# Performance work log

Hardware: AMD Instinct MI355X
Metric: run time of the kernel (lower is better)

## Reference

```python
import jax, jax.numpy as jnp
import numpy as np

N_DRUG = 20000; N_DIS = 20000; E_G = 320000
B = 4096; N_MOL = 65536; E_MOL = 262144
IN = 128; H = 256; OUT = 128; NF = 9; V = 128
EPS = 1e-5


def _bn(x, g, b):
    # BatchNorm1d in training mode: batch statistics (biased var), eps=1e-5
    m = jnp.mean(x, 0); v = jnp.var(x, 0)
    return g * (x - m) * jax.lax.rsqrt(v + EPS) + b


def _gcn_conv(x, W, b, src, dst, n):
    # PyG GCNConv: add self-loops, sym-normalized aggregation of x@W, + bias
    h = x @ W  # [n, out]
    deg = jnp.ones((n,), x.dtype).at[dst].add(jnp.ones(src.shape, x.dtype))  # deg incl. self-loop
    dinv = jax.lax.rsqrt(deg)
    msg = (dinv[src] * dinv[dst])[:, None] * h[src]  # [E, out]
    out = (h / deg[:, None]).at[dst].add(msg)  # self-loop norm = 1/deg
    return out + b


def _gcn(x, Ws, bs, gs, betas, edge_index, n):
    src, dst = edge_index[0], edge_index[1]
    for i in range(len(Ws) - 1):
        x = jax.nn.relu(_bn(_gcn_conv(x, Ws[i], bs[i], src, dst, n), gs[i], betas[i]))
    return _gcn_conv(x, Ws[-1], bs[-1], src, dst, n)


def _conv_block(x, W, b, g, beta):
    # Conv1d(k=3,s=1,p=1) -> MaxPool1d(2,2) -> BatchNorm1d -> ReLU
    y = jax.lax.conv_general_dilated(x, W, (1,), ((1, 1),), dimension_numbers=('NCH', 'OIH', 'NCH')) + b[None, :, None]
    y = jax.lax.reduce_window(y, -jnp.inf, jax.lax.max, (1, 1, 2), (1, 1, 2), 'VALID')
    m = jnp.mean(y, (0, 2)); v = jnp.var(y, (0, 2))
    y = g[None, :, None] * (y - m[None, :, None]) * jax.lax.rsqrt(v + EPS)[None, :, None] + beta[None, :, None]
    return jax.nn.relu(y)


def setup_inputs() -> dict:
    key = jax.random.key(0)
    ks = iter(jax.random.split(key, 64))
    def nrm(shape, s=0.05):
        return jax.random.normal(next(ks), shape, jnp.float32) * s
    inp = {}
    inp['drug_x'] = nrm((N_DRUG, IN), 1.0)
    inp['drug_edge_index'] = jax.random.randint(next(ks), (2, E_G), 0, N_DRUG)
    inp['drug_idx'] = jax.random.randint(next(ks), (B,), 0, N_DRUG)
    inp['dis_x'] = nrm((N_DIS, IN), 1.0)
    inp['dis_edge_index'] = jax.random.randint(next(ks), (2, E_G), 0, N_DIS)
    inp['dis_idx'] = jax.random.randint(next(ks), (B,), 0, N_DIS)
    inp['mol_x'] = jax.random.randint(next(ks), (N_MOL, NF), 0, V)
    inp['mol_edge_index'] = jax.random.randint(next(ks), (2, E_MOL), 0, N_MOL)
    inp['mol_batch'] = jnp.sort(jax.random.randint(next(ks), (N_MOL,), 0, B))
    for p in ['dr', 'di']:
        inp[p + '_W0'] = nrm((IN, H)); inp[p + '_W1'] = nrm((H, H)); inp[p + '_W2'] = nrm((H, OUT))
        inp[p + '_b0'] = jnp.zeros((H,)); inp[p + '_b1'] = jnp.zeros((H,)); inp[p + '_b2'] = jnp.zeros((OUT,))
        inp[p + '_g0'] = jnp.ones((H,)); inp[p + '_g1'] = jnp.ones((H,))
        inp[p + '_be0'] = jnp.zeros((H,)); inp[p + '_be1'] = jnp.zeros((H,))
    inp['mol_emb'] = nrm((NF, V, H))
    inp['mo_W0'] = nrm((H, H)); inp['mo_W1'] = nrm((H, H)); inp['mo_W2'] = nrm((H, OUT))
    inp['mo_b0'] = jnp.zeros((H,)); inp['mo_b1'] = jnp.zeros((H,)); inp['mo_b2'] = jnp.zeros((OUT,))
    inp['mo_g0'] = jnp.ones((H,)); inp['mo_g1'] = jnp.ones((H,))
    inp['mo_be0'] = jnp.zeros((H,)); inp['mo_be1'] = jnp.zeros((H,))
    inp['c1_W'] = nrm((6, 3, 3), 0.2); inp['c1_b'] = jnp.zeros((6,)); inp['c1_g'] = jnp.ones((6,)); inp['c1_be'] = jnp.zeros((6,))
    inp['c2_W'] = nrm((6, 6, 3), 0.2); inp['c2_b'] = jnp.zeros((6,)); inp['c2_g'] = jnp.ones((6,)); inp['c2_be'] = jnp.zeros((6,))
    inp['l1_W'] = nrm((192, 128)); inp['l1_b'] = jnp.zeros((128,))
    inp['l2_W'] = nrm((128, 1)); inp['l2_b'] = jnp.zeros((1,))
    return inp


def reference(drug_x, drug_edge_index, drug_idx, dis_x, dis_edge_index, dis_idx, mol_x, mol_edge_index, mol_batch,
              dr_W0, dr_W1, dr_W2, dr_b0, dr_b1, dr_b2, dr_g0, dr_g1, dr_be0, dr_be1,
              di_W0, di_W1, di_W2, di_b0, di_b1, di_b2, di_g0, di_g1, di_be0, di_be1,
              mol_emb, mo_W0, mo_W1, mo_W2, mo_b0, mo_b1, mo_b2, mo_g0, mo_g1, mo_be0, mo_be1,
              c1_W, c1_b, c1_g, c1_be, c2_W, c2_b, c2_g, c2_be, l1_W, l1_b, l2_W, l2_b):
    dfeat = _gcn(drug_x, [dr_W0, dr_W1, dr_W2], [dr_b0, dr_b1, dr_b2], [dr_g0, dr_g1], [dr_be0, dr_be1], drug_edge_index, N_DRUG)
    sfeat = _gcn(dis_x, [di_W0, di_W1, di_W2], [di_b0, di_b1, di_b2], [di_g0, di_g1], [di_be0, di_be1], dis_edge_index, N_DIS)
    # AtomEncoder: sum of per-feature categorical embeddings -> [N_MOL, H]
    h = jnp.sum(mol_emb[jnp.arange(NF)[None, :], mol_x], axis=1)
    mfeat = _gcn(h, [mo_W0, mo_W1, mo_W2], [mo_b0, mo_b1, mo_b2], [mo_g0, mo_g1], [mo_be0, mo_be1], mol_edge_index, N_MOL)
    mpool = jax.ops.segment_sum(mfeat, mol_batch, num_segments=B)  # global_add_pool
    fea = jnp.concatenate([dfeat[drug_idx], mpool, sfeat[dis_idx]], axis=1).reshape(B, 3, OUT)
    fea = _conv_block(fea, c1_W, c1_b, c1_g, c1_be)
    fea = _conv_block(fea, c2_W, c2_b, c2_g, c2_be)
    fea = fea.reshape(B, -1)  # [B, 192]
    fea = jax.nn.relu(fea @ l1_W + l1_b)
    return fea @ l2_W + l2_b
```

## Files before the change

kernel.cpp:

```cpp
#include <hip/hip_runtime.h>
#include <hip/hip_bf16.h>

#define N_DRUG 20000
#define N_DIS  20000
#define E_G    320000
#define BATCH  4096
#define N_MOL  65536
#define E_MOL  262144
#define DIN    128
#define DH     256
#define NF     9
#define NV     128
#define SPAN_P 20096
#define NP     40192

typedef short s16x8 __attribute__((ext_vector_type(8)));
typedef unsigned short u16x8 __attribute__((ext_vector_type(8)));
typedef float f32x4 __attribute__((ext_vector_type(4)));

typedef __attribute__((address_space(1))) const void gvoid_t;
typedef __attribute__((address_space(3))) void lvoid_t;

__device__ __forceinline__ float bfu2f(unsigned short u) {
    return __uint_as_float(((unsigned int)u) << 16);
}
__device__ __forceinline__ unsigned short f2bfu(float f) {
    __hip_bfloat16 b = __float2bfloat16(f);
    return *reinterpret_cast<unsigned short*>(&b);
}
__device__ __forceinline__ void atomAddF(float* p, float v) { unsafeAtomicAdd(p, v); }

__global__ void k_sentinel(float* out, int n, float v) {
    int i = blockIdx.x * 256 + threadIdx.x;
    if (i < n) out[i] = v;
}

__global__ void k_cast_pair(const float* __restrict__ a, const float* __restrict__ b,
                            unsigned short* __restrict__ out) {
    int i4 = blockIdx.x * 256 + threadIdx.x;
    if (i4 >= NP * 32) return;
    int row = i4 >> 5, c4 = (i4 & 31) * 4;
    float4 v = {0.f, 0.f, 0.f, 0.f};
    if (row < N_DRUG) v = *reinterpret_cast<const float4*>(a + (size_t)row * 128 + c4);
    else if (row >= SPAN_P && row < SPAN_P + N_DIS)
        v = *reinterpret_cast<const float4*>(b + (size_t)(row - SPAN_P) * 128 + c4);
    ushort4 o = {f2bfu(v.x), f2bfu(v.y), f2bfu(v.z), f2bfu(v.w)};
    *reinterpret_cast<ushort4*>(out + (size_t)row * 128 + c4) = o;
}

__global__ void k_wcast3(const float* __restrict__ W0, const float* __restrict__ W1,
                         const float* __restrict__ W2,
                         unsigned short* __restrict__ T0, unsigned short* __restrict__ T1,
                         unsigned short* __restrict__ T2, int Cin) {
    int i = blockIdx.x * 256 + threadIdx.x;
    int t0 = Cin * 256, t1 = 256 * 256, t2 = 256 * 128;
    if (i < t0) {
        int k = i / 256, c = i - k * 256;
        T0[(size_t)c * Cin + k] = f2bfu(W0[i]);
    } else if (i < t0 + t1) {
        int e = i - t0;
        int k = e / 256, c = e - k * 256;
        T1[(size_t)c * 256 + k] = f2bfu(W1[e]);
    } else if (i < t0 + t1 + t2) {
        int e = i - t0 - t1;
        int k = e / 128, c = e - k * 128;
        T2[(size_t)c * 256 + k] = f2bfu(W2[e]);
    }
}

__global__ void k_count(const int* __restrict__ dst, int* __restrict__ cnt, int E) {
    int e = blockIdx.x * 256 + threadIdx.x;
    if (e < E) atomicAdd(&cnt[dst[e]], 1);
}
__global__ void k_count2(const int* __restrict__ eiA, const int* __restrict__ eiB,
                         int* __restrict__ cnt) {
    int e = blockIdx.x * 256 + threadIdx.x;
    if (e >= 2 * E_G) return;
    int d = (e < E_G) ? eiA[E_G + e] : eiB[E_G + e - E_G] + SPAN_P;
    atomicAdd(&cnt[d], 1);
}

__global__ void k_scan1(const int* __restrict__ cnt, int* __restrict__ rowStart,
                        int* __restrict__ bsum, float* __restrict__ dinv, int n) {
    __shared__ int sh[256];
    int i = blockIdx.x * 256 + threadIdx.x;
    int v = (i < n) ? cnt[i] : 0;
    if (i < n) dinv[i] = rsqrtf(1.0f + (float)v);
    sh[threadIdx.x] = v;
    __syncthreads();
    for (int off = 1; off < 256; off <<= 1) {
        int t = (threadIdx.x >= off) ? sh[threadIdx.x - off] : 0;
        __syncthreads();
        sh[threadIdx.x] += t;
        __syncthreads();
    }
    if (i < n) rowStart[i] = sh[threadIdx.x] - v;
    if (threadIdx.x == 255) bsum[blockIdx.x] = sh[255];
}
__global__ void k_scan3(int* __restrict__ rowStart, int* __restrict__ cursor,
                        const int* __restrict__ bsum, int n, int nb, int E) {
    __shared__ int sh[256];
    int t = threadIdx.x;
    int v = (t < nb) ? bsum[t] : 0;
    sh[t] = v;
    __syncthreads();
    for (int off = 1; off < 256; off <<= 1) {
        int u = (t >= off) ? sh[t - off] : 0;
        __syncthreads();
        sh[t] += u;
        __syncthreads();
    }
    int pre = (blockIdx.x == 0) ? 0 : sh[blockIdx.x - 1];
    int i = blockIdx.x * 256 + t;
    if (i < n) {
        int r = rowStart[i] + pre;
        rowStart[i] = r;
        cursor[i] = r;
    }
    if (i == 0) rowStart[n] = E;
}
__global__ void k_fill(const int* __restrict__ src, const int* __restrict__ dst,
                       const float* __restrict__ dinv,
                       int* __restrict__ cursor, int2* __restrict__ csr2, int E) {
    int e = blockIdx.x * 256 + threadIdx.x;
    if (e < E) {
        int s = src[e], d = dst[e];
        int p = atomicAdd(&cursor[d], 1);
        csr2[p] = make_int2(s, __float_as_int(dinv[s] * dinv[d]));
    }
}
__global__ void k_fill2(const int* __restrict__ eiA, const int* __restrict__ eiB,
                        const float* __restrict__ dinv,
                        int* __restrict__ cursor, int2* __restrict__ csr2) {
    int e = blockIdx.x * 256 + threadIdx.x;
    if (e >= 2 * E_G) return;
    int s, d;
    if (e < E_G) { s = eiA[e]; d = eiA[E_G + e]; }
    else { s = eiB[e - E_G] + SPAN_P; d = eiB[E_G + e - E_G] + SPAN_P; }
    int p = atomicAdd(&cursor[d], 1);
    csr2[p] = make_int2(s, __float_as_int(dinv[s] * dinv[d]));
}

template<int AFFINE, int STATS, int BATCHED>
__global__ __launch_bounds__(256) void k_gemm_mfma(const unsigned short* __restrict__ A,
                                                   const unsigned short* __restrict__ Bt0,
                                                   const unsigned short* __restrict__ Bt1,
                                                   const float* __restrict__ coef,
                                                   unsigned short* __restrict__ Cout,
                                                   float* __restrict__ bnbuf,
                                                   int Mloc, int SPAN, int K, int N) {
    __shared__ unsigned short Al[2][4][128][8];
    __shared__ unsigned short Bl[2][4][128][8];
    __shared__ float csc[256], csh[256];
    const int tid = threadIdx.x;
    const int bm = blockIdx.y * 128;
    const int bn = blockIdx.x * 128;
    int g, lbm;
    if (BATCHED) { int tpg = SPAN >> 7; g = (int)blockIdx.y / tpg; lbm = bm - g * SPAN; }
    else { g = 0; lbm = bm; }
    const unsigned short* Bt = g ? Bt1 : Bt0;
    const int w = tid >> 6, l = tid & 63;
    const int wrow = (w >> 1) * 64, wcol = (w & 1) * 64;
    const int kg = l >> 4, lr = l & 15;

    if (AFFINE) {
        for (int i = tid; i < K; i += 256) {
            csc[i] = coef[g * 512 + i];
            csh[i] = coef[g * 512 + 256 + i];
        }
    }
    if (lbm + 128 > Mloc) {
        for (int s = tid; s < 1024; s += 256) {
            u16x8 z = {0, 0, 0, 0, 0, 0, 0, 0};
            *reinterpret_cast<u16x8*>(&Al[0][0][0][0] + s * 8) = z;
        }
    }
    __syncthreads();

    auto stage = [&](int buf, int k0) {
#pragma unroll
        for (int i = 0; i < 4; ++i) {
            int id = w * 4 + i;
            int koff = (id >> 1) & 3;
            int half = id & 1;
            int row = half * 64 + l;
            if (id < 8) {
                if (lbm + row < Mloc) {
                    const unsigned short* gs = A + (size_t)(bm + row) * K + k0 + koff * 8;
                    __builtin_amdgcn_global_load_lds((gvoid_t*)gs,
                        (lvoid_t*)&Al[buf][koff][half * 64][0], 16, 0, 0);
                }
            } else {
                const unsigned short* gs = Bt + (size_t)(bn + row) * K + k0 + koff * 8;
                __builtin_amdgcn_global_load_lds((gvoid_t*)gs,
                    (lvoid_t*)&Bl[buf][koff][half * 64][0], 16, 0, 0);
            }
        }
    };

    f32x4 acc[4][4];
#pragma unroll
    for (int fm = 0; fm < 4; ++fm)
#pragma unroll
        for (int fn = 0; fn < 4; ++fn) acc[fm][fn] = f32x4{0.f, 0.f, 0.f, 0.f};

    stage(0, 0);
    __syncthreads();
    int nk = K >> 5;
    for (int t = 0; t < nk; ++t) {
        int cur = t & 1;
        if (t + 1 < nk) stage(cur ^ 1, (t + 1) * 32);
        s16x8 a[4], b[4];
#pragma unroll
        for (int fm = 0; fm < 4; ++fm)
            a[fm] = *reinterpret_cast<const s16x8*>(&Al[cur][kg][wrow + fm * 16 + lr][0]);
        if (AFFINE) {
            int k0 = t * 32;
            float sc[8], sh[8];
#pragma unroll
            for (int e = 0; e < 8; ++e) {
                sc[e] = csc[k0 + kg * 8 + e];
                sh[e] = csh[k0 + kg * 8 + e];
            }
#pragma unroll
            for (int fm = 0; fm < 4; ++fm)
#pragma unroll
                for (int e = 0; e < 8; ++e) {
// ... 12 lines not shown
        __syncthreads();
    }
#pragma unroll
    for (int fm = 0; fm < 4; ++fm)
#pragma unroll
        for (int r = 0; r < 4; ++r) {
            int row = bm + wrow + fm * 16 + kg * 4 + r;
#pragma unroll
            for (int fn = 0; fn < 4; ++fn) {
                int col = bn + wcol + fn * 16 + lr;
                Cout[(size_t)row * N + col] = f2bfu(acc[fm][fn][r]);
            }
        }
    if constexpr (STATS) {
        __shared__ float colS[128], colQ[128];
        if (tid < 128) { colS[tid] = 0.f; colQ[tid] = 0.f; }
        __syncthreads();
#pragma unroll
        for (int fn = 0; fn < 4; ++fn) {
            float s = 0.f, q = 0.f;
#pragma unroll
            for (int fm = 0; fm < 4; ++fm)
#pragma unroll
                for (int r = 0; r < 4; ++r) {
                    float v = acc[fm][fn][r];
                    s += v; q += v * v;
                }
            int cl = (w & 1) * 64 + fn * 16 + lr;
            atomicAdd(&colS[cl], s);
            atomicAdd(&colQ[cl], q);
        }
        __syncthreads();
        if (tid < 128) {
            atomAddF(&bnbuf[g * 512 + bn + tid], colS[tid]);
            atomAddF(&bnbuf[g * 512 + 256 + bn + tid], colQ[tid]);
        }
    }
}

template<int C, int BIAS, int OUTBF>
__global__ __launch_bounds__(256) void k_gather(const unsigned short* __restrict__ h,
                                                const float* __restrict__ dinv,
                                                const float* __restrict__ bias0,
                                                const float* __restrict__ bias1,
                                                const int2* __restrict__ csr2,
                                                const int* __restrict__ rowStart,
                                                void* __restrict__ outv, int n, int SPAN) {
    constexpr int PL = C / 32;
    int row = blockIdx.x * 8 + (threadIdx.x >> 5);
    if (row >= n) return;
    int lane = threadIdx.x & 31;
    int c0 = lane * PL;

    auto loadRow = [&](int r, float* d) {
        const unsigned short* base = h + (size_t)r * C + c0;
        if constexpr (PL == 8) {
            u16x8 v = *reinterpret_cast<const u16x8*>(base);
#pragma unroll
            for (int e = 0; e < 8; ++e) d[e] = bfu2f((unsigned short)v[e]);
        } else {
            ushort4 v = *reinterpret_cast<const ushort4*>(base);
            d[0] = bfu2f(v.x); d[1] = bfu2f(v.y); d[2] = bfu2f(v.z); d[3] = bfu2f(v.w);
        }
    };

    float dd = dinv[row], ws = dd * dd;
    int beg = rowStart[row], end = rowStart[row + 1];
    float a0[PL], a1[PL], a2[PL], a3[PL], t0[PL], t1[PL], t2[PL], t3[PL];
    loadRow(row, t0);
#pragma unroll
    for (int p = 0; p < PL; ++p) { a0[p] = t0[p] * ws; a1[p] = 0.f; a2[p] = 0.f; a3[p] = 0.f; }

    int j = beg;
    for (; j + 4 <= end; j += 4) {
        int2 e0 = csr2[j], e1 = csr2[j + 1], e2 = csr2[j + 2], e3 = csr2[j + 3];
        float w0 = __int_as_float(e0.y), w1 = __int_as_float(e1.y);
        float w2 = __int_as_float(e2.y), w3 = __int_as_float(e3.y);
        loadRow(e0.x, t0); loadRow(e1.x, t1); loadRow(e2.x, t2); loadRow(e3.x, t3);
#pragma unroll
        for (int p = 0; p < PL; ++p) {
            a0[p] += w0 * t0[p]; a1[p] += w1 * t1[p];
            a2[p] += w2 * t2[p]; a3[p] += w3 * t3[p];
        }
    }
    for (; j < end; ++j) {
        int2 e0 = csr2[j];
        float w = __int_as_float(e0.y);
        loadRow(e0.x, t0);
#pragma unroll
        for (int p = 0; p < PL; ++p) a0[p] += w * t0[p];
    }
    const float* bp = (BIAS && row >= SPAN) ? bias1 : bias0;
#pragma unroll
    for (int p = 0; p < PL; ++p) {
        a0[p] += (a1[p] + a2[p]) + a3[p];
        if (BIAS) a0[p] += bp[c0 + p];
    }
    if constexpr (OUTBF) {
        unsigned short* o = (unsigned short*)outv + (size_t)row * C + c0;
        if constexpr (PL == 8) {
            u16x8 ov;
#pragma unroll
            for (int e = 0; e < 8; ++e) ov[e] = f2bfu(a0[e]);
            *reinterpret_cast<u16x8*>(o) = ov;
        } else {
            ushort4 ov = {f2bfu(a0[0]), f2bfu(a0[1]), f2bfu(a0[2]), f2bfu(a0[3])};
            *reinterpret_cast<ushort4*>(o) = ov;
        }
    } else {
        float* o = (float*)outv + (size_t)row * C + c0;
#pragma unroll
        for (int q = 0; q < PL / 4; ++q) {
            float4 ov = {a0[q * 4 + 0], a0[q * 4 + 1], a0[q * 4 + 2], a0[q * 4 + 3]};
            *reinterpret_cast<float4*>(o + q * 4) = ov;
        }
    }
}

__global__ __launch_bounds__(256) void k_bn_stats_bf(const unsigned short* __restrict__ x,
                                                     float* __restrict__ bnbuf, int SPAN) {
    __shared__ float smS[8][256];
    __shared__ float smQ[8][256];
    int t = threadIdx.x;
    int y = blockIdx.y;
    int g = t >> 5;
    int lane = t & 31;
    int c0 = lane * 8;
    float s[8], q[8];
#pragma unroll
    for (int e = 0; e < 8; ++e) { s[e] = 0.f; q[e] = 0.f; }
    int stride = gridDim.x * 8;
    for (int r = blockIdx.x * 8 + g; r < SPAN; r += stride) {
        u16x8 v = *reinterpret_cast<const u16x8*>(x + ((size_t)y * SPAN + r) * 256 + c0);
#pragma unroll
        for (int e = 0; e < 8; ++e) {
            float f = bfu2f((unsigned short)v[e]);
            s[e] += f; q[e] += f * f;
        }
    }
#pragma unroll
    for (int e = 0; e < 8; ++e) { smS[g][c0 + e] = s[e]; smQ[g][c0 + e] = q[e]; }
    __syncthreads();
    float S = 0.f, Q = 0.f;
#pragma unroll
    for (int g2 = 0; g2 < 8; ++g2) { S += smS[g2][t]; Q += smQ[g2][t]; }
    atomAddF(&bnbuf[y * 512 + t], S);
    atomAddF(&bnbuf[y * 512 + 256 + t], Q);
}

__global__ void k_bn_coef(float* __restrict__ bnbuf,
                          const float* __restrict__ gA, const float* __restrict__ beA,
                          const float* __restrict__ gB, const float* __restrict__ beB,
                          float* __restrict__ coef, float invN) {
    int gg = blockIdx.x;
    int j = threadIdx.x;
    const float* gp = gg ? gB : gA;
    const float* bp = gg ? beB : beA;
    float* s = bnbuf + gg * 512;
    float m = s[j] * invN;
    float v = s[256 + j] * invN - m * m;
    float r = rsqrtf(fmaxf(v, 0.f) + 1e-5f);
    float sc = gp[j] * r;
    coef[gg * 512 + j] = sc;
    coef[gg * 512 + 256 + j] = bp[j] - m * sc;
    s[j] = 0.f;
    s[256 + j] = 0.f;
}

__global__ __launch_bounds__(256) void k_atom_enc(const int* __restrict__ mol_x,
                                                  const float* __restrict__ emb,
                                                  unsigned short* __restrict__ h) {
    __shared__ int sidx[4][NF];
    int t = threadIdx.x;
    if (t < 4 * NF) sidx[t / NF][t % NF] = mol_x[(blockIdx.x * 4 + t / NF) * NF + t % NF];
    __syncthreads();
    int r = t >> 6, lane = t & 63;
    int c0 = lane * 4;
    int row = blockIdx.x * 4 + r;
    float4 s = {0.f, 0.f, 0.f, 0.f};
#pragma unroll
    for (int f = 0; f < NF; ++f) {
        const float4 v = *reinterpret_cast<const float4*>(emb + ((size_t)f * NV + sidx[r][f]) * DH + c0);
        s.x += v.x; s.y += v.y; s.z += v.z; s.w += v.w;
    }
    ushort4 ov = {f2bfu(s.x), f2bfu(s.y), f2bfu(s.z), f2bfu(s.w)};
    *reinterpret_cast<ushort4*>(h + (size_t)row * DH + c0) = ov;
}

__global__ __launch_bounds__(128) void k_pool_seg(const unsigned short* __restrict__ mfeat,
                                                  const int* __restrict__ batch,
                                                  float* __restrict__ mpool) {
    __shared__ int sr[2];
    __shared__ float smS[8][128];
    int b = blockIdx.x, t = threadIdx.x;
    if (t < 2) {
        int target = b + t;
        int lo = 0, hi = N_MOL;
        while (lo < hi) {
            int mid = (lo + hi) >> 1;
            if (batch[mid] < target) lo = mid + 1; else hi = mid;
        }
        sr[t] = lo;
    }
    __syncthreads();
    int g = t >> 4;
    int lane = t & 15;
    int c0 = lane * 8;
    float s[8];
#pragma unroll
    for (int e = 0; e < 8; ++e) s[e] = 0.f;
    int e1 = sr[1];
    for (int i = sr[0] + g; i < e1; i += 8) {
        u16x8 v = *reinterpret_cast<const u16x8*>(mfeat + (size_t)i * 128 + c0);
#pragma unroll
        for (int e = 0; e < 8; ++e) s[e] += bfu2f((unsigned short)v[e]);
    }
#pragma unroll
    for (int e = 0; e < 8; ++e) smS[g][c0 + e] = s[e];
    __syncthreads();
    float S = 0.f;
#pragma unroll
    for (int g2 = 0; g2 < 8; ++g2) S += smS[g2][t];
    mpool[(size_t)b * 128 + t] = S;
}

__global__ __launch_bounds__(64) void k_conv1(const float* __restrict__ dfeat,
                                              const float* __restrict__ mpool,
                                              const float* __restrict__ sfeat,
                                              const int* __restrict__ drug_idx,
                                              const int* __restrict__ dis_idx,
                                              const float* __restrict__ W,
                                              const float* __restrict__ bias,
                                              float* __restrict__ y1) {
    __shared__ float xs[3][128];
    __shared__ float w[54];
    __shared__ float bb[6];
    int b = blockIdx.x, t = threadIdx.x;
    int di = drug_idx[b], si = dis_idx[b];
    const float* r0 = dfeat + (size_t)di * 128;
    const float* r1 = mpool + (size_t)b * 128;
    const float* r2 = sfeat + (size_t)si * 128;
    xs[0][t] = r0[t]; xs[0][t + 64] = r0[t + 64];
    xs[1][t] = r1[t]; xs[1][t + 64] = r1[t + 64];
    xs[2][t] = r2[t]; xs[2][t + 64] = r2[t + 64];
    if (t < 54) w[t] = W[t];
    if (t < 6) bb[t] = bias[t];
    __syncthreads();
    int l0 = 2 * t, l1 = l0 + 1;
// ... 102 lines not shown
                                              const float* __restrict__ l1b,
                                              const float* __restrict__ l2W,
                                              const float* __restrict__ l2b,
                                              float* __restrict__ out) {
    __shared__ float fs[192];
    __shared__ float sm[2];
    int b = blockIdx.x, t = threadIdx.x;
    const float* mean = hb + 32 + 16;
    const float* rstd = hb + 32 + 24;
    for (int idx = t; idx < 192; idx += 128) {
        int o = idx >> 5, l = idx & 31;
        float v = y2[((size_t)b * 6 + o) * 32 + l];
        v = g2[o] * (v - mean[o]) * rstd[o] + be2[o];
        fs[idx] = fmaxf(v, 0.f);
    }
    __syncthreads();
    float h = l1b[t];
    for (int k = 0; k < 192; ++k)
        h += fs[k] * l1W[k * 128 + t];
    h = fmaxf(h, 0.f);
    float p = h * l2W[t];
#pragma unroll
    for (int off = 32; off > 0; off >>= 1) p += __shfl_down(p, off);
    if ((t & 63) == 0) sm[t >> 6] = p;
    __syncthreads();
    if (t == 0) out[b] = sm[0] + sm[1] + l2b[0];
}

extern "C" void kernel_launch(void* const* d_in, const int* in_sizes, int n_in,
                              void* d_out, int out_size, void* d_ws, size_t ws_size,
                              hipStream_t stream) {
    float* out = (float*)d_out;
    if (n_in != 52) { k_sentinel<<<16, 256, 0, stream>>>(out, out_size, -111.f); return; }
    if (in_sizes[0] != N_DRUG * DIN || in_sizes[29] != NF * NV * DH || in_sizes[48] != 192 * 128) {
        k_sentinel<<<16, 256, 0, stream>>>(out, out_size, -222.f); return;
    }

    char* w = (char*)d_ws;
    auto alloc = [&](size_t bytes) { char* p = w; w += (bytes + 255) & ~(size_t)255; return p; };
    unsigned short* xb    = (unsigned short*)alloc((size_t)N_MOL * 256 * 2);
    unsigned short* h_bf  = (unsigned short*)alloc((size_t)N_MOL * 256 * 2);
    unsigned short* xin   = (unsigned short*)alloc((size_t)N_MOL * 256 * 2);
    float* outDS = (float*)alloc((size_t)NP * 128 * 4);
    float* mpool = (float*)alloc((size_t)BATCH * 128 * 4);
    int*   cnt      = (int*)alloc((size_t)N_MOL * 4);
    float* dinv     = (float*)alloc((size_t)N_MOL * 4);
    int*   rowStart = (int*)alloc((size_t)(N_MOL + 1) * 4);
    int*   cursor   = (int*)alloc((size_t)N_MOL * 4);
    int2*  csr2     = (int2*)alloc((size_t)(2 * E_G) * 8);
    int*   bsum     = (int*)alloc(512 * 4);
    float* bnbuf    = (float*)alloc(1024 * 4);
    float* coef     = (float*)alloc(1024 * 4);
    unsigned short* wtA0 = (unsigned short*)alloc((size_t)256 * 256 * 2);
    unsigned short* wtA1 = (unsigned short*)alloc((size_t)256 * 256 * 2);
    unsigned short* wtA2 = (unsigned short*)alloc((size_t)256 * 256 * 2);
    unsigned short* wtB0 = (unsigned short*)alloc((size_t)256 * 256 * 2);
    unsigned short* wtB1 = (unsigned short*)alloc((size_t)256 * 256 * 2);
    unsigned short* wtB2 = (unsigned short*)alloc((size_t)256 * 256 * 2);
    float* hstat = (float*)alloc(64 * 4);
    float* y1    = (float*)alloc((size_t)BATCH * 6 * 64 * 4);
    float* y2    = (float*)alloc((size_t)BATCH * 6 * 32 * 4);
    if ((size_t)(w - (char*)d_ws) > ws_size) {
        k_sentinel<<<16, 256, 0, stream>>>(out, out_size, -333.f); return;
    }

    const float* drug_x  = (const float*)d_in[0];
    const int* drug_ei   = (const int*)d_in[1];
    const int* drug_idx  = (const int*)d_in[2];
    const float* dis_x   = (const float*)d_in[3];
    const int* dis_ei    = (const int*)d_in[4];
    const int* dis_idx   = (const int*)d_in[5];
    const int* mol_x     = (const int*)d_in[6];
    const int* mol_ei    = (const int*)d_in[7];
    const int* mol_b     = (const int*)d_in[8];
    const float *dr_W0 = (const float*)d_in[9], *dr_W1 = (const float*)d_in[10], *dr_W2 = (const float*)d_in[11];
    const float *dr_b2 = (const float*)d_in[14];
    const float *dr_g0 = (const float*)d_in[15], *dr_g1 = (const float*)d_in[16];
    const float *dr_be0 = (const float*)d_in[17], *dr_be1 = (const float*)d_in[18];
    const float *di_W0 = (const float*)d_in[19], *di_W1 = (const float*)d_in[20], *di_W2 = (const float*)d_in[21];
    const float *di_b2 = (const float*)d_in[24];
    const float *di_g0 = (const float*)d_in[25], *di_g1 = (const float*)d_in[26];
    const float *di_be0 = (const float*)d_in[27], *di_be1 = (const float*)d_in[28];
    const float* mol_emb = (const float*)d_in[29];
    const float *mo_W0 = (const float*)d_in[30], *mo_W1 = (const float*)d_in[31], *mo_W2 = (const float*)d_in[32];
    const float *mo_b2 = (const float*)d_in[35];
    const float *mo_g0 = (const float*)d_in[36], *mo_g1 = (const float*)d_in[37];
    const float *mo_be0 = (const float*)d_in[38], *mo_be1 = (const float*)d_in[39];
    const float *c1_W = (const float*)d_in[40], *c1_b = (const float*)d_in[41];
    const float *c1_g = (const float*)d_in[42], *c1_be = (const float*)d_in[43];
    const float *c2_W = (const float*)d_in[44], *c2_b = (const float*)d_in[45];
    const float *c2_g = (const float*)d_in[46], *c2_be = (const float*)d_in[47];
    const float *l1_W = (const float*)d_in[48], *l1_b = (const float*)d_in[49];
    const float *l2_W = (const float*)d_in[50], *l2_b = (const float*)d_in[51];

    hipMemsetAsync(bnbuf, 0, 1024 * sizeof(float), stream);
    float invNP = 1.0f / (float)N_DRUG;
    float invNM = 1.0f / (float)N_MOL;

    k_cast_pair<<<(NP * 32 + 255) / 256, 256, 0, stream>>>(drug_x, dis_x, xin);
    hipMemsetAsync(cnt, 0, (size_t)NP * sizeof(int), stream);
    k_count2<<<(2 * E_G + 255) / 256, 256, 0, stream>>>(drug_ei, dis_ei, cnt);
    int nbP = (NP + 255) / 256;
    k_scan1<<<nbP, 256, 0, stream>>>(cnt, rowStart, bsum, dinv, NP);
    k_scan3<<<nbP, 256, 0, stream>>>(rowStart, cursor, bsum, NP, nbP, 2 * E_G);
    k_fill2<<<(2 * E_G + 255) / 256, 256, 0, stream>>>(drug_ei, dis_ei, dinv, cursor, csr2);
    int wtot = 128 * 256 + 256 * 256 + 256 * 128;
    k_wcast3<<<(wtot + 255) / 256, 256, 0, stream>>>(dr_W0, dr_W1, dr_W2, wtA0, wtA1, wtA2, 128);
    k_wcast3<<<(wtot + 255) / 256, 256, 0, stream>>>(di_W0, di_W1, di_W2, wtB0, wtB1, wtB2, 128);

    int gbP = NP / 8;
    int tyP = NP / 128;
    k_gather<128, 0, 1><<<gbP, 256, 0, stream>>>(xin, dinv, nullptr, nullptr, csr2, rowStart, xb, NP, SPAN_P);
    k_gemm_mfma<0, 1, 1><<<dim3(2, tyP), 256, 0, stream>>>(xb, wtA0, wtB0, nullptr, h_bf, bnbuf, N_DRUG, SPAN_P, 128, 256);
    k_bn_coef<<<2, 256, 0, stream>>>(bnbuf, dr_g0, dr_be0, di_g0, di_be0, coef, invNP);
    k_gemm_mfma<1, 0, 1><<<dim3(2, tyP), 256, 0, stream>>>(h_bf, wtA1, wtB1, coef, xb, nullptr, N_DRUG, SPAN_P, 256, 256);
    k_gather<256, 0, 1><<<gbP, 256, 0, stream>>>(xb, dinv, nullptr, nullptr, csr2, rowStart, h_bf, NP, SPAN_P);
    k_bn_stats_bf<<<dim3(256, 2), 256, 0, stream>>>(h_bf, bnbuf, SPAN_P);
    k_bn_coef<<<2, 256, 0, stream>>>(bnbuf, dr_g1, dr_be1, di_g1, di_be1, coef, invNP);
    k_gemm_mfma<1, 0, 1><<<dim3(1, tyP), 256, 0, stream>>>(h_bf, wtA2, wtB2, coef, xb, nullptr, N_DRUG, SPAN_P, 256, 128);
    k_gather<128, 1, 0><<<gbP, 256, 0, stream>>>(xb, dinv, dr_b2, di_b2, csr2, rowStart, outDS, NP, SPAN_P);

    k_atom_enc<<<N_MOL / 4, 256, 0, stream>>>(mol_x, mol_emb, xin);
    hipMemsetAsync(cnt, 0, (size_t)N_MOL * sizeof(int), stream);
    k_count<<<(E_MOL + 255) / 256, 256, 0, stream>>>(mol_ei + E_MOL, cnt, E_MOL);
    int nbM = N_MOL / 256;
    k_scan1<<<nbM, 256, 0, stream>>>(cnt, rowStart, bsum, dinv, N_MOL);
    k_scan3<<<nbM, 256, 0, stream>>>(rowStart, cursor, bsum, N_MOL, nbM, E_MOL);
    k_fill<<<(E_MOL + 255) / 256, 256, 0, stream>>>(mol_ei, mol_ei + E_MOL, dinv, cursor, csr2, E_MOL);
    int wtotM = 256 * 256 + 256 * 256 + 256 * 128;
    k_wcast3<<<(wtotM + 255) / 256, 256, 0, stream>>>(mo_W0, mo_W1, mo_W2, wtA0, wtA1, wtA2, 256);

    int gbM = N_MOL / 8;
    int tyM = N_MOL / 128;
    k_gather<256, 0, 1><<<gbM, 256, 0, stream>>>(xin, dinv, nullptr, nullptr, csr2, rowStart, xb, N_MOL, N_MOL);
    k_gemm_mfma<0, 1, 0><<<dim3(2, tyM), 256, 0, stream>>>(xb, wtA0, wtA0, nullptr, h_bf, bnbuf, N_MOL, N_MOL, 256, 256);
    k_bn_coef<<<1, 256, 0, stream>>>(bnbuf, mo_g0, mo_be0, mo_g0, mo_be0, coef, invNM);
    k_gemm_mfma<1, 0, 0><<<dim3(2, tyM), 256, 0, stream>>>(h_bf, wtA1, wtA1, coef, xb, nullptr, N_MOL, N_MOL, 256, 256);
    k_gather<256, 0, 1><<<gbM, 256, 0, stream>>>(xb, dinv, nullptr, nullptr, csr2, rowStart, h_bf, N_MOL, N_MOL);
    k_bn_stats_bf<<<dim3(256, 1), 256, 0, stream>>>(h_bf, bnbuf, N_MOL);
    k_bn_coef<<<1, 256, 0, stream>>>(bnbuf, mo_g1, mo_be1, mo_g1, mo_be1, coef, invNM);
    k_gemm_mfma<1, 0, 0><<<dim3(1, tyM), 256, 0, stream>>>(h_bf, wtA2, wtA2, coef, xb, nullptr, N_MOL, N_MOL, 256, 128);
    k_gather<128, 1, 1><<<gbM, 256, 0, stream>>>(xb, dinv, mo_b2, mo_b2, csr2, rowStart, h_bf, N_MOL, N_MOL);
    k_pool_seg<<<BATCH, 128, 0, stream>>>(h_bf, mol_b, mpool);

    const float* dfeat = outDS;
    const float* sfeat = outDS + (size_t)SPAN_P * 128;
    hipMemsetAsync(hstat, 0, 64 * 4, stream);
    k_conv1<<<BATCH, 64, 0, stream>>>(dfeat, mpool, sfeat, drug_idx, dis_idx, c1_W, c1_b, y1);
    k_head_stats<<<dim3(6, BATCH / 256), 256, 0, stream>>>(y1, hstat, 0, 64);
    k_bn_fin<<<1, 8, 0, stream>>>(hstat, 0, 1.0f / (BATCH * 64.0f));
    k_conv2<<<BATCH, 64, 0, stream>>>(y1, hstat, c1_g, c1_be, c2_W, c2_b, y2);
    k_head_stats<<<dim3(6, BATCH / 256), 256, 0, stream>>>(y2, hstat, 1, 32);
    k_bn_fin<<<1, 8, 0, stream>>>(hstat, 1, 1.0f / (BATCH * 32.0f));
    k_head<<<BATCH, 128, 0, stream>>>(y2, hstat, c2_g, c2_be, l1_W, l1_b, l2_W, l2_b, out);
}
```

Before: 596.2 us.

## Batch drug, disease and molecule GCNs into shared launches over a concatenated graph

Concatenates the drug, disease and molecule graphs into one node and edge space so CSR build, gathers, GEMMs and BN stats/coef run as combined launches covering all three GCNs. This cuts the number of kernel launches and lets the small drug/disease work overlap with the larger molecule work instead of running serially. The final layer output now stays in fp32 for all graphs, so pooling reads float instead of bf16, which adds memory traffic. The combined scan also adds a separate block-sum scan kernel.

Measured after the change: 561.8 us. 5.8% less time.

```diff
diff --git a/kernel.cpp b/kernel.cpp
--- a/kernel.cpp
+++ b/kernel.cpp
@@ -7,12 +7,13 @@
 #define BATCH  4096
 #define N_MOL  65536
 #define E_MOL  262144
-#define DIN    128
-#define DH     256
 #define NF     9
 #define NV     128
+#define DH     256
 #define SPAN_P 20096
 #define NP     40192
+#define NTOT   105728
+#define ETOT   902144
 
 typedef short s16x8 __attribute__((ext_vector_type(8)));
 typedef unsigned short u16x8 __attribute__((ext_vector_type(8)));
@@ -68,15 +69,14 @@
     }
 }
 
-__global__ void k_count(const int* __restrict__ dst, int* __restrict__ cnt, int E) {
+__global__ void k_count3(const int* __restrict__ eA, const int* __restrict__ eB,
+                         const int* __restrict__ eC, int* __restrict__ cnt) {
     int e = blockIdx.x * 256 + threadIdx.x;
-    if (e < E) atomicAdd(&cnt[dst[e]], 1);
-}
-__global__ void k_count2(const int* __restrict__ eiA, const int* __restrict__ eiB,
-                         int* __restrict__ cnt) {
-    int e = blockIdx.x * 256 + threadIdx.x;
-    if (e >= 2 * E_G) return;
-    int d = (e < E_G) ? eiA[E_G + e] : eiB[E_G + e - E_G] + SPAN_P;
+    if (e >= ETOT) return;
+    int d;
+    if (e < E_G) d = eA[E_G + e];
+    else if (e < 2 * E_G) d = eB[E_G + (e - E_G)] + SPAN_P;
+    else d = eC[E_MOL + (e - 2 * E_G)] + NP;
     atomicAdd(&cnt[d], 1);
 }
 
@@ -97,76 +97,83 @@
     if (i < n) rowStart[i] = sh[threadIdx.x] - v;
     if (threadIdx.x == 255) bsum[blockIdx.x] = sh[255];
 }
+__global__ void k_scan2b(int* __restrict__ bsum, int nb) {
+    __shared__ int sh[256];
+    __shared__ int carry;
+    int t = threadIdx.x;
+    if (t == 0) carry = 0;
+    __syncthreads();
+    for (int c0 = 0; c0 < nb; c0 += 256) {
+        int v = (c0 + t < nb) ? bsum[c0 + t] : 0;
+        sh[t] = v;
+        __syncthreads();
+        for (int off = 1; off < 256; off <<= 1) {
+            int u = (t >= off) ? sh[t - off] : 0;
+            __syncthreads();
+            sh[t] += u;
+            __syncthreads();
+        }
+        if (c0 + t < nb) bsum[c0 + t] = carry + sh[t] - v;
+        __syncthreads();
+        if (t == 0) carry += sh[255];
+        __syncthreads();
+    }
+}
 __global__ void k_scan3(int* __restrict__ rowStart, int* __restrict__ cursor,
-                        const int* __restrict__ bsum, int n, int nb, int E) {
-    __shared__ int sh[256];
-    int t = threadIdx.x;
-    int v = (t < nb) ? bsum[t] : 0;
-    sh[t] = v;
-    __syncthreads();
-    for (int off = 1; off < 256; off <<= 1) {
-        int u = (t >= off) ? sh[t - off] : 0;
-        __syncthreads();
-        sh[t] += u;
-        __syncthreads();
-    }
-    int pre = (blockIdx.x == 0) ? 0 : sh[blockIdx.x - 1];
-    int i = blockIdx.x * 256 + t;
+                        const int* __restrict__ bsum, int n, int E) {
+    int i = blockIdx.x * 256 + threadIdx.x;
     if (i < n) {
-        int r = rowStart[i] + pre;
+        int r = rowStart[i] + bsum[blockIdx.x];
         rowStart[i] = r;
         cursor[i] = r;
     }
     if (i == 0) rowStart[n] = E;
 }
-__global__ void k_fill(const int* __restrict__ src, const int* __restrict__ dst,
-                       const float* __restrict__ dinv,
-                       int* __restrict__ cursor, int2* __restrict__ csr2, int E) {
-    int e = blockIdx.x * 256 + threadIdx.x;
-    if (e < E) {
-        int s = src[e], d = dst[e];
-        int p = atomicAdd(&cursor[d], 1);
-        csr2[p] = make_int2(s, __float_as_int(dinv[s] * dinv[d]));
-    }
-}
-__global__ void k_fill2(const int* __restrict__ eiA, const int* __restrict__ eiB,
-                        const float* __restrict__ dinv,
+__global__ void k_fill3(const int* __restrict__ eA, const int* __restrict__ eB,
+                        const int* __restrict__ eC, const float* __restrict__ dinv,
                         int* __restrict__ cursor, int2* __restrict__ csr2) {
     int e = blockIdx.x * 256 + threadIdx.x;
-    if (e >= 2 * E_G) return;
+    if (e >= ETOT) return;
     int s, d;
-    if (e < E_G) { s = eiA[e]; d = eiA[E_G + e]; }
-    else { s = eiB[e - E_G] + SPAN_P; d = eiB[E_G + e - E_G] + SPAN_P; }
+    if (e < E_G) { s = eA[e]; d = eA[E_G + e]; }
+    else if (e < 2 * E_G) { int i = e - E_G; s = eB[i] + SPAN_P; d = eB[E_G + i] + SPAN_P; }
+    else { int i = e - 2 * E_G; s = eC[i] + NP; d = eC[E_MOL + i] + NP; }
     int p = atomicAdd(&cursor[d], 1);
     csr2[p] = make_int2(s, __float_as_int(dinv[s] * dinv[d]));
 }
 
-template<int AFFINE, int STATS, int BATCHED>
+template<int AFFINE, int STATS>
 __global__ __launch_bounds__(256) void k_gemm_mfma(const unsigned short* __restrict__ A,
                                                    const unsigned short* __restrict__ Bt0,
                                                    const unsigned short* __restrict__ Bt1,
+                                                   const unsigned short* __restrict__ Bt2,
                                                    const float* __restrict__ coef,
                                                    unsigned short* __restrict__ Cout,
                                                    float* __restrict__ bnbuf,
-                                                   int Mloc, int SPAN, int K, int N) {
+                                                   int tb0, int tb1, int off1, int off2,
+                                                   int m0, int m1, int m2, int gbase,
+                                                   int K, int N) {
     __shared__ unsigned short Al[2][4][128][8];
     __shared__ unsigned short Bl[2][4][128][8];
     __shared__ float csc[256], csh[256];
     const int tid = threadIdx.x;
-    const int bm = blockIdx.y * 128;
+    const int y = blockIdx.y;
+    const int bm = y * 128;
     const int bn = blockIdx.x * 128;
-    int g, lbm;
-    if (BATCHED) { int tpg = SPAN >> 7; g = (int)blockIdx.y / tpg; lbm = bm - g * SPAN; }
-    else { g = 0; lbm = bm; }
-    const unsigned short* Bt = g ? Bt1 : Bt0;
+    const int g = (y >= tb1) ? 2 : ((y >= tb0) ? 1 : 0);
+    const int off = (g == 0) ? 0 : ((g == 1) ? off1 : off2);
+    const int Mloc = (g == 0) ? m0 : ((g == 1) ? m1 : m2);
+    const int lbm = bm - off;
+    const unsigned short* Bt = (g == 0) ? Bt0 : ((g == 1) ? Bt1 : Bt2);
+    const int gs = gbase + g;
     const int w = tid >> 6, l = tid & 63;
     const int wrow = (w >> 1) * 64, wcol = (w & 1) * 64;
     const int kg = l >> 4, lr = l & 15;
 
     if (AFFINE) {
         for (int i = tid; i < K; i += 256) {
-            csc[i] = coef[g * 512 + i];
-            csh[i] = coef[g * 512 + 256 + i];
+            csc[i] = coef[gs * 512 + i];
+            csh[i] = coef[gs * 512 + 256 + i];
         }
     }
     if (lbm + 128 > Mloc) {
@@ -186,13 +193,13 @@
             int row = half * 64 + l;
             if (id < 8) {
                 if (lbm + row < Mloc) {
-                    const unsigned short* gs = A + (size_t)(bm + row) * K + k0 + koff * 8;
-                    __builtin_amdgcn_global_load_lds((gvoid_t*)gs,
+                    const unsigned short* gsrc = A + (size_t)(bm + row) * K + k0 + koff * 8;
+                    __builtin_amdgcn_global_load_lds((gvoid_t*)gsrc,
                         (lvoid_t*)&Al[buf][koff][half * 64][0], 16, 0, 0);
                 }
             } else {
-                const unsigned short* gs = Bt + (size_t)(bn + row) * K + k0 + koff * 8;
-                __builtin_amdgcn_global_load_lds((gvoid_t*)gs,
+                const unsigned short* gsrc = Bt + (size_t)(bn + row) * K + k0 + koff * 8;
+                __builtin_amdgcn_global_load_lds((gvoid_t*)gsrc,
                     (lvoid_t*)&Bl[buf][koff][half * 64][0], 16, 0, 0);
             }
         }
@@ -271,28 +278,31 @@
         }
         __syncthreads();
         if (tid < 128) {
-            atomAddF(&bnbuf[g * 512 + bn + tid], colS[tid]);
-            atomAddF(&bnbuf[g * 512 + 256 + bn + tid], colQ[tid]);
+            atomAddF(&bnbuf[gs * 512 + bn + tid], colS[tid]);
+            atomAddF(&bnbuf[gs * 512 + 256 + bn + tid], colQ[tid]);
         }
     }
 }
 
 template<int C, int BIAS, int OUTBF>
 __global__ __launch_bounds__(256) void k_gather(const unsigned short* __restrict__ h,
+                                                long long hoff,
                                                 const float* __restrict__ dinv,
-                                                const float* __restrict__ bias0,
-                                                const float* __restrict__ bias1,
+                                                const float* __restrict__ b0,
+                                                const float* __restrict__ b1,
+                                                const float* __restrict__ b2,
                                                 const int2* __restrict__ csr2,
                                                 const int* __restrict__ rowStart,
-                                                void* __restrict__ outv, int n, int SPAN) {
+                                                void* __restrict__ outv, long long ooff,
+                                                int rowoff, int rowend) {
     constexpr int PL = C / 32;
-    int row = blockIdx.x * 8 + (threadIdx.x >> 5);
-    if (row >= n) return;
+    int row = rowoff + blockIdx.x * 8 + (threadIdx.x >> 5);
+    if (row >= rowend) return;
     int lane = threadIdx.x & 31;
     int c0 = lane * PL;
 
     auto loadRow = [&](int r, float* d) {
-        const unsigned short* base = h + (size_t)r * C + c0;
+        const unsigned short* base = h + ((size_t)r * C - hoff) + c0;
         if constexpr (PL == 8) {
             u16x8 v = *reinterpret_cast<const u16x8*>(base);
 #pragma unroll
@@ -329,14 +339,15 @@
 #pragma unroll
         for (int p = 0; p < PL; ++p) a0[p] += w * t0[p];
     }
-    const float* bp = (BIAS && row >= SPAN) ? bias1 : bias0;
+    const float* bp = nullptr;
+    if (BIAS) bp = (row < SPAN_P) ? b0 : ((row < NP) ? b1 : b2);
 #pragma unroll
     for (int p = 0; p < PL; ++p) {
         a0[p] += (a1[p] + a2[p]) + a3[p];
         if (BIAS) a0[p] += bp[c0 + p];
     }
     if constexpr (OUTBF) {
-        unsigned short* o = (unsigned short*)outv + (size_t)row * C + c0;
+        unsigned short* o = (unsigned short*)outv + ((size_t)row * C - ooff) + c0;
         if constexpr (PL == 8) {
             u16x8 ov;
 #pragma unroll
@@ -347,7 +358,7 @@
             *reinterpret_cast<ushort4*>(o) = ov;
         }
     } else {
-        float* o = (float*)outv + (size_t)row * C + c0;
+        float* o = (float*)outv + ((size_t)row * C - ooff) + c0;
 #pragma unroll
         for (int q = 0; q < PL / 4; ++q) {
             float4 ov = {a0[q * 4 + 0], a0[q * 4 + 1], a0[q * 4 + 2], a0[q * 4 + 3]};
@@ -356,12 +367,14 @@
     }
 }
 
-__global__ __launch_bounds__(256) void k_bn_stats_bf(const unsigned short* __restrict__ x,
-                                                     float* __restrict__ bnbuf, int SPAN) {
+__global__ __launch_bounds__(256) void k_bn_stats3(const unsigned short* __restrict__ x,
+                                                   float* __restrict__ bnbuf) {
     __shared__ float smS[8][256];
     __shared__ float smQ[8][256];
     int t = threadIdx.x;
     int y = blockIdx.y;
+    int off = (y < 2) ? y * SPAN_P : NP;
+    int span = (y < 2) ? SPAN_P : N_MOL;
     int g = t >> 5;
     int lane = t & 31;
     int c0 = lane * 8;
@@ -369,8 +382,8 @@
 #pragma unroll
     for (int e = 0; e < 8; ++e) { s[e] = 0.f; q[e] = 0.f; }
     int stride = gridDim.x * 8;
-    for (int r = blockIdx.x * 8 + g; r < SPAN; r += stride) {
-        u16x8 v = *reinterpret_cast<const u16x8*>(x + ((size_t)y * SPAN + r) * 256 + c0);
+    for (int r = blockIdx.x * 8 + g; r < span; r += stride) {
+        u16x8 v = *reinterpret_cast<const u16x8*>(x + ((size_t)(off + r)) * 256 + c0);
 #pragma unroll
         for (int e = 0; e < 8; ++e) {
             float f = bfu2f((unsigned short)v[e]);
@@ -387,14 +400,16 @@
     atomAddF(&bnbuf[y * 512 + 256 + t], Q);
 }
 
-__global__ void k_bn_coef(float* __restrict__ bnbuf,
-                          const float* __restrict__ gA, const float* __restrict__ beA,
-                          const float* __restrict__ gB, const float* __restrict__ beB,
-                          float* __restrict__ coef, float invN) {
+__global__ void k_bn_coef3(float* __restrict__ bnbuf,
+                           const float* __restrict__ g0, const float* __restrict__ be0,
+                           const float* __restrict__ g1, const float* __restrict__ be1,
+                           const float* __restrict__ g2, const float* __restrict__ be2,
+                           float* __restrict__ coef, float invN01, float invN2) {
     int gg = blockIdx.x;
     int j = threadIdx.x;
-    const float* gp = gg ? gB : gA;
-    const float* bp = gg ? beB : beA;
+    const float* gp = (gg == 0) ? g0 : ((gg == 1) ? g1 : g2);
+    const float* bp = (gg == 0) ? be0 : ((gg == 1) ? be1 : be2);
+    float invN = (gg < 2) ? invN01 : invN2;
     float* s = bnbuf + gg * 512;
     float m = s[j] * invN;
     float v = s[256 + j] * invN - m * m;
@@ -426,9 +441,9 @@
     *reinterpret_cast<ushort4*>(h + (size_t)row * DH + c0) = ov;
 }
 
-__global__ __launch_bounds__(128) void k_pool_seg(const unsigned short* __restrict__ mfeat,
-                                                  const int* __restrict__ batch,
-                                                  float* __restrict__ mpool) {
+__global__ __launch_bounds__(128) void k_pool_seg_f(const float* __restrict__ mfeat,
+                                                    const int* __restrict__ batch,
+                                                    float* __restrict__ mpool) {
     __shared__ int sr[2];
     __shared__ float smS[8][128];
     int b = blockIdx.x, t = threadIdx.x;
@@ -450,9 +465,10 @@
     for (int e = 0; e < 8; ++e) s[e] = 0.f;
     int e1 = sr[1];
     for (int i = sr[0] + g; i < e1; i += 8) {
-        u16x8 v = *reinterpret_cast<const u16x8*>(mfeat + (size_t)i * 128 + c0);
-#pragma unroll
-        for (int e = 0; e < 8; ++e) s[e] += bfu2f((unsigned short)v[e]);
+        const float4 v0 = *reinterpret_cast<const float4*>(mfeat + (size_t)i * 128 + c0);
+        const float4 v1 = *reinterpret_cast<const float4*>(mfeat + (size_t)i * 128 + c0 + 4);
+        s[0] += v0.x; s[1] += v0.y; s[2] += v0.z; s[3] += v0.w;
+        s[4] += v1.x; s[5] += v1.y; s[6] += v1.z; s[7] += v1.w;
     }
 #pragma unroll
     for (int e = 0; e < 8; ++e) smS[g][c0 + e] = s[e];
@@ -621,31 +637,33 @@
                               hipStream_t stream) {
     float* out = (float*)d_out;
     if (n_in != 52) { k_sentinel<<<16, 256, 0, stream>>>(out, out_size, -111.f); return; }
-    if (in_sizes[0] != N_DRUG * DIN || in_sizes[29] != NF * NV * DH || in_sizes[48] != 192 * 128) {
+    if (in_sizes[0] != N_DRUG * 128 || in_sizes[29] != NF * NV * DH || in_sizes[48] != 192 * 128) {
         k_sentinel<<<16, 256, 0, stream>>>(out, out_size, -222.f); return;
     }
 
     char* w = (char*)d_ws;
     auto alloc = [&](size_t bytes) { char* p = w; w += (bytes + 255) & ~(size_t)255; return p; };
-    unsigned short* xb    = (unsigned short*)alloc((size_t)N_MOL * 256 * 2);
-    unsigned short* h_bf  = (unsigned short*)alloc((size_t)N_MOL * 256 * 2);
-    unsigned short* xin   = (unsigned short*)alloc((size_t)N_MOL * 256 * 2);
-    float* outDS = (float*)alloc((size_t)NP * 128 * 4);
+    unsigned short* B1 = (unsigned short*)alloc((size_t)NTOT * 256 * 2);
+    unsigned short* B2 = (unsigned short*)alloc((size_t)NTOT * 256 * 2);
+    float* fcat = (float*)B1;
     float* mpool = (float*)alloc((size_t)BATCH * 128 * 4);
-    int*   cnt      = (int*)alloc((size_t)N_MOL * 4);
-    float* dinv     = (float*)alloc((size_t)N_MOL * 4);
-    int*   rowStart = (int*)alloc((size_t)(N_MOL + 1) * 4);
-    int*   cursor   = (int*)alloc((size_t)N_MOL * 4);
-    int2*  csr2     = (int2*)alloc((size_t)(2 * E_G) * 8);
-    int*   bsum     = (int*)alloc(512 * 4);
-    float* bnbuf    = (float*)alloc(1024 * 4);
-    float* coef     = (float*)alloc(1024 * 4);
-    unsigned short* wtA0 = (unsigned short*)alloc((size_t)256 * 256 * 2);
-    unsigned short* wtA1 = (unsigned short*)alloc((size_t)256 * 256 * 2);
-    unsigned short* wtA2 = (unsigned short*)alloc((size_t)256 * 256 * 2);
-    unsigned short* wtB0 = (unsigned short*)alloc((size_t)256 * 256 * 2);
-    unsigned short* wtB1 = (unsigned short*)alloc((size_t)256 * 256 * 2);
-    unsigned short* wtB2 = (unsigned short*)alloc((size_t)256 * 256 * 2);
+    int*   cnt      = (int*)alloc((size_t)NTOT * 4);
+    float* dinv     = (float*)alloc((size_t)NTOT * 4);
+    int*   rowStart = (int*)alloc((size_t)(NTOT + 1) * 4);
+    int*   cursor   = (int*)alloc((size_t)NTOT * 4);
+    int2*  csr2     = (int2*)alloc((size_t)ETOT * 8);
+    int*   bsum     = (int*)alloc(1024 * 4);
+    float* bnbuf    = (float*)alloc(1536 * 4);
+    float* coef     = (float*)alloc(1536 * 4);
+    unsigned short* drT0 = (unsigned short*)alloc((size_t)128 * 256 * 2);
+    unsigned short* drT1 = (unsigned short*)alloc((size_t)256 * 256 * 2);
+    unsigned short* drT2 = (unsigned short*)alloc((size_t)256 * 128 * 2);
+    unsigned short* diT0 = (unsigned short*)alloc((size_t)128 * 256 * 2);
+    unsigned short* diT1 = (unsigned short*)alloc((size_t)256 * 256 * 2);
+    unsigned short* diT2 = (unsigned short*)alloc((size_t)256 * 128 * 2);
+    unsigned short* moT0 = (unsigned short*)alloc((size_t)256 * 256 * 2);
+    unsigned short* moT1 = (unsigned short*)alloc((size_t)256 * 256 * 2);
+    unsigned short* moT2 = (unsigned short*)alloc((size_t)256 * 128 * 2);
     float* hstat = (float*)alloc(64 * 4);
     float* y1    = (float*)alloc((size_t)BATCH * 6 * 64 * 4);
     float* y2    = (float*)alloc((size_t)BATCH * 6 * 32 * 4);
@@ -682,58 +700,55 @@
     const float *l1_W = (const float*)d_in[48], *l1_b = (const float*)d_in[49];
     const float *l2_W = (const float*)d_in[50], *l2_b = (const float*)d_in[51];
 
-    hipMemsetAsync(bnbuf, 0, 1024 * sizeof(float), stream);
-    float invNP = 1.0f / (float)N_DRUG;
-    float invNM = 1.0f / (float)N_MOL;
-
-    k_cast_pair<<<(NP * 32 + 255) / 256, 256, 0, stream>>>(drug_x, dis_x, xin);
-    hipMemsetAsync(cnt, 0, (size_t)NP * sizeof(int), stream);
-    k_count2<<<(2 * E_G + 255) / 256, 256, 0, stream>>>(drug_ei, dis_ei, cnt);
-    int nbP = (NP + 255) / 256;
-    k_scan1<<<nbP, 256, 0, stream>>>(cnt, rowStart, bsum, dinv, NP);
-    k_scan3<<<nbP, 256, 0, stream>>>(rowStart, cursor, bsum, NP, nbP, 2 * E_G);
-    k_fill2<<<(2 * E_G + 255) / 256, 256, 0, stream>>>(drug_ei, dis_ei, dinv, cursor, csr2);
-    int wtot = 128 * 256 + 256 * 256 + 256 * 128;
-    k_wcast3<<<(wtot + 255) / 256, 256, 0, stream>>>(dr_W0, dr_W1, dr_W2, wtA0, wtA1, wtA2, 128);
-    k_wcast3<<<(wtot + 255) / 256, 256, 0, stream>>>(di_W0, di_W1, di_W2, wtB0, wtB1, wtB2, 128);
-
-    int gbP = NP / 8;
-    int tyP = NP / 128;
-    k_gather<128, 0, 1><<<gbP, 256, 0, stream>>>(xin, dinv, nullptr, nullptr, csr2, rowStart, xb, NP, SPAN_P);
-    k_gemm_mfma<0, 1, 1><<<dim3(2, tyP), 256, 0, stream>>>(xb, wtA0, wtB0, nullptr, h_bf, bnbuf, N_DRUG, SPAN_P, 128, 256);
-    k_bn_coef<<<2, 256, 0, stream>>>(bnbuf, dr_g0, dr_be0, di_g0, di_be0, coef, invNP);
-    k_gemm_mfma<1, 0, 1><<<dim3(2, tyP), 256, 0, stream>>>(h_bf, wtA1, wtB1, coef, xb, nullptr, N_DRUG, SPAN_P, 256, 256);
-    k_gather<256, 0, 1><<<gbP, 256, 0, stream>>>(xb, dinv, nullptr, nullptr, csr2, rowStart, h_bf, NP, SPAN_P);
-    k_bn_stats_bf<<<dim3(256, 2), 256, 0, stream>>>(h_bf, bnbuf, SPAN_P);
-    k_bn_coef<<<2, 256, 0, stream>>>(bnbuf, dr_g1, dr_be1, di_g1, di_be1, coef, invNP);
-    k_gemm_mfma<1, 0, 1><<<dim3(1, tyP), 256, 0, stream>>>(h_bf, wtA2, wtB2, coef, xb, nullptr, N_DRUG, SPAN_P, 256, 128);
-    k_gather<128, 1, 0><<<gbP, 256, 0, stream>>>(xb, dinv, dr_b2, di_b2, csr2, rowStart, outDS, NP, SPAN_P);
-
-    k_atom_enc<<<N_MOL / 4, 256, 0, stream>>>(mol_x, mol_emb, xin);
-    hipMemsetAsync(cnt, 0, (size_t)N_MOL * sizeof(int), stream);
-    k_count<<<(E_MOL + 255) / 256, 256, 0, stream>>>(mol_ei + E_MOL, cnt, E_MOL);
-    int nbM = N_MOL / 256;
-    k_scan1<<<nbM, 256, 0, stream>>>(cnt, rowStart, bsum, dinv, N_MOL);
-    k_scan3<<<nbM, 256, 0, stream>>>(rowStart, cursor, bsum, N_MOL, nbM, E_MOL);
-    k_fill<<<(E_MOL + 255) / 256, 256, 0, stream>>>(mol_ei, mol_ei + E_MOL, dinv, cursor, csr2, E_MOL);
-    int wtotM = 256 * 256 + 256 * 256 + 256 * 128;
-    k_wcast3<<<(wtotM + 255) / 256, 256, 0, stream>>>(mo_W0, mo_W1, mo_W2, wtA0, wtA1, wtA2, 256);
-
-    int gbM = N_MOL / 8;
-    int tyM = N_MOL / 128;
-    k_gather<256, 0, 1><<<gbM, 256, 0, stream>>>(xin, dinv, nullptr, nullptr, csr2, rowStart, xb, N_MOL, N_MOL);
-    k_gemm_mfma<0, 1, 0><<<dim3(2, tyM), 256, 0, stream>>>(xb, wtA0, wtA0, nullptr, h_bf, bnbuf, N_MOL, N_MOL, 256, 256);
-    k_bn_coef<<<1, 256, 0, stream>>>(bnbuf, mo_g0, mo_be0, mo_g0, mo_be0, coef, invNM);
-    k_gemm_mfma<1, 0, 0><<<dim3(2, tyM), 256, 0, stream>>>(h_bf, wtA1, wtA1, coef, xb, nullptr, N_MOL, N_MOL, 256, 256);
-    k_gather<256, 0, 1><<<gbM, 256, 0, stream>>>(xb, dinv, nullptr, nullptr, csr2, rowStart, h_bf, N_MOL, N_MOL);
-    k_bn_stats_bf<<<dim3(256, 1), 256, 0, stream>>>(h_bf, bnbuf, N_MOL);
-    k_bn_coef<<<1, 256, 0, stream>>>(bnbuf, mo_g1, mo_be1, mo_g1, mo_be1, coef, invNM);
-    k_gemm_mfma<1, 0, 0><<<dim3(1, tyM), 256, 0, stream>>>(h_bf, wtA2, wtA2, coef, xb, nullptr, N_MOL, N_MOL, 256, 128);
-    k_gather<128, 1, 1><<<gbM, 256, 0, stream>>>(xb, dinv, mo_b2, mo_b2, csr2, rowStart, h_bf, N_MOL, N_MOL);
-    k_pool_seg<<<BATCH, 128, 0, stream>>>(h_bf, mol_b, mpool);
-
-    const float* dfeat = outDS;
-    const float* sfeat = outDS + (size_t)SPAN_P * 128;
+    const float invN01 = 1.0f / (float)N_DRUG;
+    const float invNM  = 1.0f / (float)N_MOL;
+    const long long MOFF = (long long)NP * 128;
+
+    hipMemsetAsync(bnbuf, 0, 1536 * sizeof(float), stream);
+
+    k_cast_pair<<<(NP * 32 + 255) / 256, 256, 0, stream>>>(drug_x, dis_x, B1);
+    k_atom_enc<<<N_MOL / 4, 256, 0, stream>>>(mol_x, mol_emb, B1 + MOFF);
+
+    hipMemsetAsync(cnt, 0, (size_t)NTOT * sizeof(int), stream);
+    k_count3<<<(ETOT + 255) / 256, 256, 0, stream>>>(drug_ei, dis_ei, mol_ei, cnt);
+    int nb = (NTOT + 255) / 256;
+    k_scan1<<<nb, 256, 0, stream>>>(cnt, rowStart, bsum, dinv, NTOT);
+    k_scan2b<<<1, 256, 0, stream>>>(bsum, nb);
+    k_scan3<<<nb, 256, 0, stream>>>(rowStart, cursor, bsum, NTOT, ETOT);
+    k_fill3<<<(ETOT + 255) / 256, 256, 0, stream>>>(drug_ei, dis_ei, mol_ei, dinv, cursor, csr2);
+
+    int wt1 = 128 * 256 + 256 * 256 + 256 * 128;
+    int wt2 = 256 * 256 + 256 * 256 + 256 * 128;
+    k_wcast3<<<(wt1 + 255) / 256, 256, 0, stream>>>(dr_W0, dr_W1, dr_W2, drT0, drT1, drT2, 128);
+    k_wcast3<<<(wt1 + 255) / 256, 256, 0, stream>>>(di_W0, di_W1, di_W2, diT0, diT1, diT2, 128);
+    k_wcast3<<<(wt2 + 255) / 256, 256, 0, stream>>>(mo_W0, mo_W1, mo_W2, moT0, moT1, moT2, 256);
+
+    const int BIG = 1 << 28;
+    k_gather<128, 0, 1><<<NP / 8, 256, 0, stream>>>(B1, 0, dinv, nullptr, nullptr, nullptr,
+                                                    csr2, rowStart, B2, 0, 0, NP);
+    k_gather<256, 0, 1><<<N_MOL / 8, 256, 0, stream>>>(B1, MOFF, dinv, nullptr, nullptr, nullptr,
+                                                       csr2, rowStart, B2, MOFF, NP, NTOT);
+    k_gemm_mfma<0, 1><<<dim3(2, 314), 256, 0, stream>>>(B2, drT0, diT0, nullptr, nullptr,
+        B1, bnbuf, 157, BIG, SPAN_P, 0, N_DRUG, N_DIS, 0, 0, 128, 256);
+    k_gemm_mfma<0, 1><<<dim3(2, 512), 256, 0, stream>>>(B2 + MOFF, moT0, nullptr, nullptr, nullptr,
+        B1 + (size_t)NP * 256, bnbuf, BIG, BIG, 0, 0, N_MOL, 0, 0, 2, 256, 256);
+    k_bn_coef3<<<3, 256, 0, stream>>>(bnbuf, dr_g0, dr_be0, di_g0, di_be0, mo_g0, mo_be0,
+                                      coef, invN01, invNM);
+    k_gemm_mfma<1, 0><<<dim3(2, 826), 256, 0, stream>>>(B1, drT1, diT1, moT1, coef,
+        B2, nullptr, 157, 314, SPAN_P, NP, N_DRUG, N_DIS, N_MOL, 0, 256, 256);
+    k_gather<256, 0, 1><<<NTOT / 8, 256, 0, stream>>>(B2, 0, dinv, nullptr, nullptr, nullptr,
+                                                      csr2, rowStart, B1, 0, 0, NTOT);
+    k_bn_stats3<<<dim3(256, 3), 256, 0, stream>>>(B1, bnbuf);
+    k_bn_coef3<<<3, 256, 0, stream>>>(bnbuf, dr_g1, dr_be1, di_g1, di_be1, mo_g1, mo_be1,
+                                      coef, invN01, invNM);
+    k_gemm_mfma<1, 0><<<dim3(1, 826), 256, 0, stream>>>(B1, drT2, diT2, moT2, coef,
+        B2, nullptr, 157, 314, SPAN_P, NP, N_DRUG, N_DIS, N_MOL, 0, 256, 128);
+    k_gather<128, 1, 0><<<NTOT / 8, 256, 0, stream>>>(B2, 0, dinv, dr_b2, di_b2, mo_b2,
+                                                      csr2, rowStart, fcat, 0, 0, NTOT);
+    k_pool_seg_f<<<BATCH, 128, 0, stream>>>(fcat + (size_t)NP * 128, mol_b, mpool);
+
+    const float* dfeat = fcat;
+    const float* sfeat = fcat + (size_t)SPAN_P * 128;
     hipMemsetAsync(hstat, 0, 64 * 4, stream);
     k_conv1<<<BATCH, 64, 0, stream>>>(dfeat, mpool, sfeat, drug_idx, dis_idx, c1_W, c1_b, y1);
     k_head_stats<<<dim3(6, BATCH / 256), 256, 0, stream>>>(y1, hstat, 0, 64);
```
